# Kernel optimization log

Measured on AMD Instinct MI355X. Metric: run time of the kernel, lower is better.

The kernel has to match this reference:

```python
import jax, jax.numpy as jnp
import numpy as np

DEGREE = 8
HIDDEN = 256
IN_DIM = 3
N_LAYERS = 8  # num_hidden_layers=8 -> 1 input + 6 middle + 1 output ChebyKAN layers


def cheby_layer(x, coeff):
    """x: [P, in], coeff: [in, out, degree+1] -> [P, out].
    Computes tanh(x), Chebyshev recurrence T_0..T_d, and contracts
    sum_d T_d(x)_i * coeff[i, o, d] without materializing the full basis.
    """
    x = jnp.tanh(x)
    t_prev = jnp.ones_like(x)          # T_0
    t_cur = x                          # T_1
    out = jnp.einsum('pi,io->po', t_prev, coeff[:, :, 0])
    out = out + jnp.einsum('pi,io->po', t_cur, coeff[:, :, 1])
    for d in range(2, coeff.shape[-1]):
        t_prev, t_cur = t_cur, 2.0 * x * t_cur - t_prev
        out = out + jnp.einsum('pi,io->po', t_cur, coeff[:, :, d])
    return out


def decode(pts, ws):
    h = pts
    for w in ws:
        h = cheby_layer(h, w)
    return h


def setup_inputs() -> dict:
    key = jax.random.key(0)
    k_nm, k_m, *k_ws = jax.random.split(key, 2 + N_LAYERS)
    B, N = 4, 16384
    inp = {
        'non_mnfld_pnts': jax.random.normal(k_nm, (B, N, IN_DIM), dtype=jnp.float32),
        'mnfld_pnts': jax.random.normal(k_m, (B, N, IN_DIM), dtype=jnp.float32),
    }
    dims = [IN_DIM] + [HIDDEN] * (N_LAYERS - 1) + [1]
    for i in range(N_LAYERS):
        fan_in, fan_out = dims[i], dims[i + 1]
        std = 1.0 / (fan_in * (DEGREE + 1))
        inp[f'w{i}'] = jax.random.normal(k_ws[i], (fan_in, fan_out, DEGREE + 1), dtype=jnp.float32) * std
    return inp


def reference(non_mnfld_pnts, mnfld_pnts, w0, w1, w2, w3, w4, w5, w6, w7):
    ws = [w0, w1, w2, w3, w4, w5, w6, w7]
    B = non_mnfld_pnts.shape[0]
    mnfld_pred = decode(mnfld_pnts.reshape(-1, IN_DIM), ws).reshape(B, -1)
    nonmnfld_pred = decode(non_mnfld_pnts.reshape(-1, IN_DIM), ws).reshape(B, -1)
    return (mnfld_pred, nonmnfld_pred)
```

## Files before the change

kernel.cpp:

```cpp
#include <hip/hip_runtime.h>

typedef _Float16 f16;
typedef __attribute__((ext_vector_type(4)))  _Float16 f16x4;
typedef __attribute__((ext_vector_type(8)))  _Float16 f16x8;
typedef __attribute__((ext_vector_type(16))) float    f32x16;

#define WT_L (8*256*256)

__device__ __forceinline__ float fexp2(float x) {
#if __has_builtin(__builtin_amdgcn_exp2f)
    return __builtin_amdgcn_exp2f(x);
#else
    return exp2f(x);
#endif
}

__device__ __forceinline__ float fast_tanh(float v) {
    float a = __builtin_fabsf(v);
    float e = fexp2(a * -2.8853900817779268f);
    float r = (1.0f - e) * __builtin_amdgcn_rcpf(1.0f + e);
    return __builtin_copysignf(r, v);
}

__global__ void prep_all(const float* __restrict__ w0, const float* __restrict__ w1,
                         const float* __restrict__ w2, const float* __restrict__ w3,
                         const float* __restrict__ w4, const float* __restrict__ w5,
                         const float* __restrict__ w6, const float* __restrict__ w7,
                         f16* __restrict__ wt, float* __restrict__ biasp,
                         float* __restrict__ w0t, float* __restrict__ w7p)
{
    __shared__ float red[256];
    const int bi = blockIdx.x, t = threadIdx.x;
    if (bi < 1536) {
        const int L = bi >> 8, o = bi & 255, i = t;
        const float* w;
        switch (L) { case 0: w = w1; break; case 1: w = w2; break; case 2: w = w3; break;
                     case 3: w = w4; break; case 4: w = w5; break; default: w = w6; }
        float v[9];
#pragma unroll
        for (int d = 0; d < 9; d++) v[d] = w[(i*256 + o)*9 + d];
        const int ck = i >> 4, k = i & 15;
        const int wv4 = o >> 6, nt = (o >> 5) & 1, l31 = o & 31;
        const int lane = (k >> 3)*32 + l31, e = k & 7;
        const int base = ck*4096 + wv4*1024 + nt*512 + lane*8 + e;
#pragma unroll
        for (int d = 1; d < 9; d++)
            wt[L*WT_L + (d-1)*16*4096 + base] = (f16)v[d];
        red[i] = v[0];
        __syncthreads();
#pragma unroll
        for (int s = 128; s > 0; s >>= 1) {
            if (i < s) red[i] += red[i + s];
            __syncthreads();
        }
        if (i == 0) biasp[L*256 + o] = red[0];
    } else if (bi < 1563) {
        int id = (bi - 1536)*256 + t;
        int i = id / 2304, rem = id % 2304;
        int o = rem / 9, d = rem % 9;
        w0t[(i*9 + d)*256 + o] = w0[id];
    } else {
        int id = (bi - 1563)*256 + t;
        int ch = id / 9, d = id % 9;
        w7p[ch*12 + d] = w7[id];
    }
}

__global__ void k0(const float* __restrict__ nonm, const float* __restrict__ mnf,
                   const float* __restrict__ w0t, f16* __restrict__ xg) {
    const int t = threadIdx.x, b = blockIdx.x;
    const int pt = t & 63;
    const int oh = (t >> 6) * 64;
    const int pid = b*64 + pt;
    const float* src = (pid < 65536) ? mnf : nonm;
    const int sp = (pid < 65536) ? pid : pid - 65536;
    float c0 = src[sp*3 + 0];
    float c1 = src[sp*3 + 1];
    float c2 = src[sp*3 + 2];
    float xx[3] = {fast_tanh(c0), fast_tanh(c1), fast_tanh(c2)};
    float bas[27];
#pragma unroll
    for (int i = 0; i < 3; i++) {
        float t0 = 1.0f, t1 = xx[i];
        bas[i*9+0] = t0; bas[i*9+1] = t1;
        float x2 = xx[i] + xx[i];
#pragma unroll
        for (int d = 2; d < 9; d++) {
            float t2 = x2*t1 - t0;
            bas[i*9+d] = t2; t0 = t1; t1 = t2;
        }
    }
#pragma unroll 1
    for (int q = 0; q < 16; q++) {
        int o = oh + q*4;
        float4 a = {0.f, 0.f, 0.f, 0.f};
#pragma unroll
        for (int k = 0; k < 27; k++) {
            float4 wv = *(const float4*)(w0t + k*256 + o);
            a.x = fmaf(bas[k], wv.x, a.x);
            a.y = fmaf(bas[k], wv.y, a.y);
            a.z = fmaf(bas[k], wv.z, a.z);
            a.w = fmaf(bas[k], wv.w, a.w);
        }
        f16x4 hv = {(f16)fast_tanh(a.x), (f16)fast_tanh(a.y),
                    (f16)fast_tanh(a.z), (f16)fast_tanh(a.w)};
        *(f16x4*)(xg + (size_t)pid*256 + o) = hv;
    }
}

__global__ __launch_bounds__(256, 2)
void k_mid(const f16* __restrict__ wl, const float* __restrict__ biasL,
           f16* __restrict__ xg)
{
    __shared__ __align__(16) f16 xs[128*256];

    const int t    = threadIdx.x;
    const int b    = blockIdx.x;
    const int lane = t & 63;
    const int w    = t >> 6;
    const int l31  = lane & 31;
    const int half = lane >> 5;
    const int nb   = w * 64;
    const size_t tile_off = (size_t)b * 128 * 256;

#pragma unroll
    for (int i = 0; i < 16; i++) {
        int idx = i*256 + t;
        int pt = idx >> 5, cu = idx & 31;
        f16x8 v = *(const f16x8*)(xg + tile_off + (size_t)idx*8);
        *(f16x8*)(xs + pt*256 + ((cu ^ (pt & 7))*8)) = v;
    }
    __syncthreads();

    f32x16 acc[4][2];
    const f16x8 ones = {(f16)1.f,(f16)1.f,(f16)1.f,(f16)1.f,(f16)1.f,(f16)1.f,(f16)1.f,(f16)1.f};

    const f16* wbase = wl + w*1024 + lane*8;
    float b0 = biasL[nb + l31];
    float b1 = biasL[nb + 32 + l31];
#pragma unroll
    for (int mt = 0; mt < 4; mt++)
#pragma unroll
        for (int r = 0; r < 16; r++) { acc[mt][0][r] = b0; acc[mt][1][r] = b1; }

    f16x8 xv[4], Bb[4][2];
#pragma unroll
    for (int mt = 0; mt < 4; mt++) {
        int m = mt*32 + l31;
        int unit = half ^ (m & 7);
        xv[mt] = *(const f16x8*)(xs + m*256 + unit*8);
    }
#pragma unroll
    for (int j = 0; j < 4; j++) {
        Bb[j][0] = *(const f16x8*)(wbase + j*16*4096);
        Bb[j][1] = *(const f16x8*)(wbase + j*16*4096 + 512);
    }

    f16x8 x2[4], t1[4], t0[4];
#pragma unroll 1
    for (int ck = 0; ck < 16; ck++) {
        const int ckn = (ck < 15) ? ck + 1 : 15;
#pragma unroll
        for (int mt = 0; mt < 4; mt++) {
            t1[mt] = xv[mt];
            x2[mt] = xv[mt] + xv[mt];
            t0[mt] = ones;
        }
#pragma unroll
        for (int mt = 0; mt < 4; mt++) {
            int m = mt*32 + l31;
            int unit = (ckn*2 + half) ^ (m & 7);
            xv[mt] = *(const f16x8*)(xs + m*256 + unit*8);
        }
#pragma unroll
        for (int j = 0; j < 8; j++) {
            const int ck2 = (j < 4) ? ck : ckn;
            const int j2  = (j < 4) ? (j + 4) : (j - 4);
            const int off = (j2*16 + ck2)*4096;
            f16x8 pb0 = *(const f16x8*)(wbase + off);
            f16x8 pb1 = *(const f16x8*)(wbase + off + 512);
#pragma unroll
            for (int mt = 0; mt < 4; mt++) {
                acc[mt][0] = __builtin_amdgcn_mfma_f32_32x32x16_f16(t1[mt], Bb[j&3][0], acc[mt][0], 0, 0, 0);
                acc[mt][1] = __builtin_amdgcn_mfma_f32_32x32x16_f16(t1[mt], Bb[j&3][1], acc[mt][1], 0, 0, 0);
            }
            if (j < 7) {
#pragma unroll
                for (int mt = 0; mt < 4; mt++) {
                    f16x8 tn = x2[mt]*t1[mt] - t0[mt];
                    t0[mt] = t1[mt];
                    t1[mt] = tn;
                }
            }
            Bb[j&3][0] = pb0;
            Bb[j&3][1] = pb1;
        }
    }
    __syncthreads();

#pragma unroll
    for (int mt = 0; mt < 4; mt++) {
#pragma unroll
        for (int nt = 0; nt < 2; nt++) {
            int ch = nb + nt*32 + l31;
            int cu = ch >> 3, ce = ch & 7;
#pragma unroll
            for (int r = 0; r < 16; r++) {
                int p = mt*32 + (r & 3) + 8*(r >> 2) + 4*half;
                int unit = cu ^ (p & 7);
                xs[p*256 + unit*8 + ce] = (f16)fast_tanh(acc[mt][nt][r]);
            }
        }
    }
    __syncthreads();

#pragma unroll
    for (int i = 0; i < 16; i++) {
        int idx = i*256 + t;
        int pt = idx >> 5, cu = idx & 31;
        f16x8 v = *(const f16x8*)(xs + pt*256 + ((cu ^ (pt & 7))*8));
        *(f16x8*)(xg + tile_off + (size_t)idx*8) = v;
    }
}

__global__ void k7(const f16* __restrict__ xg, const float* __restrict__ w7p,
                   float* __restrict__ out) {
    __shared__ float w7s[256*12];
    const int t = threadIdx.x, b = blockIdx.x;
#pragma unroll
    for (int i = 0; i < 12; i++) w7s[i*256 + t] = w7p[i*256 + t];
    __syncthreads();
    const int pid = b*256 + t;
    const f16* row = xg + (size_t)pid*256;
    float s = 0.0f;
#pragma unroll 1
    for (int cu = 0; cu < 32; cu++) {
        f16x8 xv = *(const f16x8*)(row + cu*8);
#pragma unroll
        for (int e = 0; e < 8; e++) {
            int ch = cu*8 + e;
            const float* wr = w7s + ch*12;
            float x = (float)xv[e];
            float x2 = x + x;
            float t0 = 1.0f, t1v = x;
            s = fmaf(wr[0], t0, s);
            s = fmaf(wr[1], t1v, s);
            float t2 = x2*t1v - t0;  s = fmaf(wr[2], t2, s);
            float t3 = x2*t2 - t1v;  s = fmaf(wr[3], t3, s);
            float t4 = x2*t3 - t2;   s = fmaf(wr[4], t4, s);
            float t5 = x2*t4 - t3;   s = fmaf(wr[5], t5, s);
            float t6 = x2*t5 - t4;   s = fmaf(wr[6], t6, s);
            float t7 = x2*t6 - t5;   s = fmaf(wr[7], t7, s);
            float t8 = x2*t7 - t6;   s = fmaf(wr[8], t8, s);
        }
    }
    out[pid] = s;
}

extern "C" void kernel_launch(void* const* d_in, const int* in_sizes, int n_in,
                              void* d_out, int out_size, void* d_ws, size_t ws_size,
                              hipStream_t stream) {
    const float* nonm = (const float*)d_in[0];
    const float* mnf  = (const float*)d_in[1];

    char* ws = (char*)d_ws;
    f16*   wtp   = (f16*)ws;
    float* biasp = (float*)(ws + 6*WT_L*2);
    float* w0tp  = (float*)(ws + 6*WT_L*2 + 6144);
    float* w7pp  = (float*)(ws + 6*WT_L*2 + 6144 + 27648);
    f16*   xg    = (f16*)(ws + 6*WT_L*2 + 6144 + 27648 + 12288);

    prep_all<<<1572, 256, 0, stream>>>((const float*)d_in[2], (const float*)d_in[3],
                                       (const float*)d_in[4], (const float*)d_in[5],
                                       (const float*)d_in[6], (const float*)d_in[7],
                                       (const float*)d_in[8], (const float*)d_in[9],
                                       wtp, biasp, w0tp, w7pp);

    k0<<<2048, 256, 0, stream>>>(nonm, mnf, w0tp, xg);
    for (int L = 0; L < 6; L++)
        k_mid<<<1024, 256, 0, stream>>>(wtp + L*WT_L, biasp + L*256, xg);
    k7<<<512, 256, 0, stream>>>(xg, w7pp, (float*)d_out);
}
```

Before: 1.003 ms.

## Stream mid-layer weights through LDS with async global_load_lds and coalesce k0 stores

New measurement: 1.114 ms. 11.0% more time.

```diff
diff --git a/kernel.cpp b/kernel.cpp
--- a/kernel.cpp
+++ b/kernel.cpp
@@ -6,6 +6,15 @@
 typedef __attribute__((ext_vector_type(16))) float    f32x16;
 
 #define WT_L (8*256*256)
+
+#define WAIT_VM2   0x0F72
+#define WAIT_VM0   0x0F70
+#define WAIT_LGKM0 0xC07F
+
+__device__ __forceinline__ void async_b16(const f16* g, f16* l) {
+    __builtin_amdgcn_global_load_lds((const __attribute__((address_space(1))) void*)g,
+                                     (__attribute__((address_space(3))) void*)l, 16, 0, 0);
+}
 
 __device__ __forceinline__ float fexp2(float x) {
 #if __has_builtin(__builtin_amdgcn_exp2f)
@@ -68,6 +77,7 @@
 
 __global__ void k0(const float* __restrict__ nonm, const float* __restrict__ mnf,
                    const float* __restrict__ w0t, f16* __restrict__ xg) {
+    __shared__ __align__(16) f16 sh[64*256];
     const int t = threadIdx.x, b = blockIdx.x;
     const int pt = t & 63;
     const int oh = (t >> 6) * 64;
@@ -104,8 +114,21 @@
         }
         f16x4 hv = {(f16)fast_tanh(a.x), (f16)fast_tanh(a.y),
                     (f16)fast_tanh(a.z), (f16)fast_tanh(a.w)};
-        *(f16x4*)(xg + (size_t)pid*256 + o) = hv;
-    }
+        int unit = (o >> 3) ^ (pt & 7);
+        *(f16x4*)(sh + pt*256 + unit*8 + (o & 7)) = hv;
+    }
+    __syncthreads();
+#pragma unroll
+    for (int i = 0; i < 8; i++) {
+        int idx = i*256 + t;
+        int p2 = idx >> 5, cu = idx & 31;
+        f16x8 v = *(const f16x8*)(sh + p2*256 + ((cu ^ (p2 & 7))*8));
+        *(f16x8*)(xg + (size_t)b*16384 + (size_t)idx*8) = v;
+    }
+}
+
+__device__ __forceinline__ int goff(int s) {
+    return ((s & 7)*16 + (s >> 3)) * 4096;
 }
 
 __global__ __launch_bounds__(256, 2)
@@ -113,6 +136,7 @@
            f16* __restrict__ xg)
 {
     __shared__ __align__(16) f16 xs[128*256];
+    __shared__ __align__(16) f16 bring[2*4*1024];
 
     const int t    = threadIdx.x;
     const int b    = blockIdx.x;
@@ -121,7 +145,7 @@
     const int l31  = lane & 31;
     const int half = lane >> 5;
     const int nb   = w * 64;
-    const size_t tile_off = (size_t)b * 128 * 256;
+    const size_t tile_off = (size_t)b * 32768;
 
 #pragma unroll
     for (int i = 0; i < 16; i++) {
@@ -135,7 +159,10 @@
     f32x16 acc[4][2];
     const f16x8 ones = {(f16)1.f,(f16)1.f,(f16)1.f,(f16)1.f,(f16)1.f,(f16)1.f,(f16)1.f,(f16)1.f};
 
-    const f16* wbase = wl + w*1024 + lane*8;
+    const f16* wgl = wl + w*1024 + lane*8;
+    f16* lws = bring + w*1024;
+    const f16* lrd = bring + w*1024 + lane*8;
+
     float b0 = biasL[nb + l31];
     float b1 = biasL[nb + 32 + l31];
 #pragma unroll
@@ -143,28 +170,43 @@
 #pragma unroll
         for (int r = 0; r < 16; r++) { acc[mt][0][r] = b0; acc[mt][1][r] = b1; }
 
-    f16x8 xv[4], Bb[4][2];
+    f16x8 Bf[4][2];
+    async_b16(wgl + goff(0),       lws);
+    async_b16(wgl + goff(0) + 512, lws + 512);
+    async_b16(wgl + goff(1),       lws + 4096);
+    async_b16(wgl + goff(1) + 512, lws + 4096 + 512);
+    __builtin_amdgcn_s_waitcnt(WAIT_VM2);
+    __builtin_amdgcn_sched_barrier(0);
+    Bf[0][0] = *(const f16x8*)(lrd);
+    Bf[0][1] = *(const f16x8*)(lrd + 512);
+    __builtin_amdgcn_s_waitcnt(WAIT_VM0);
+    __builtin_amdgcn_sched_barrier(0);
+    Bf[1][0] = *(const f16x8*)(lrd + 4096);
+    Bf[1][1] = *(const f16x8*)(lrd + 4096 + 512);
+    __builtin_amdgcn_s_waitcnt(WAIT_LGKM0);
+    __builtin_amdgcn_sched_barrier(0);
+    async_b16(wgl + goff(2),       lws);
+    async_b16(wgl + goff(2) + 512, lws + 512);
+    async_b16(wgl + goff(3),       lws + 4096);
+    async_b16(wgl + goff(3) + 512, lws + 4096 + 512);
+
+    f16x8 xv[4];
 #pragma unroll
     for (int mt = 0; mt < 4; mt++) {
         int m = mt*32 + l31;
         int unit = half ^ (m & 7);
         xv[mt] = *(const f16x8*)(xs + m*256 + unit*8);
     }
-#pragma unroll
-    for (int j = 0; j < 4; j++) {
-        Bb[j][0] = *(const f16x8*)(wbase + j*16*4096);
-        Bb[j][1] = *(const f16x8*)(wbase + j*16*4096 + 512);
-    }
-
-    f16x8 x2[4], t1[4], t0[4];
+
+    f16x8 x2[4], t1[4], t0v[4];
 #pragma unroll 1
     for (int ck = 0; ck < 16; ck++) {
         const int ckn = (ck < 15) ? ck + 1 : 15;
 #pragma unroll
         for (int mt = 0; mt < 4; mt++) {
-            t1[mt] = xv[mt];
-            x2[mt] = xv[mt] + xv[mt];
-            t0[mt] = ones;
+            t1[mt]  = xv[mt];
+            x2[mt]  = xv[mt] + xv[mt];
+            t0v[mt] = ones;
         }
 #pragma unroll
         for (int mt = 0; mt < 4; mt++) {
@@ -173,27 +215,37 @@
             xv[mt] = *(const f16x8*)(xs + m*256 + unit*8);
         }
 #pragma unroll
-        for (int j = 0; j < 8; j++) {
-            const int ck2 = (j < 4) ? ck : ckn;
-            const int j2  = (j < 4) ? (j + 4) : (j - 4);
-            const int off = (j2*16 + ck2)*4096;
-            f16x8 pb0 = *(const f16x8*)(wbase + off);
-            f16x8 pb1 = *(const f16x8*)(wbase + off + 512);
+        for (int dm = 0; dm < 8; dm++) {
+            const int s = ck*8 + dm;
+            if (s + 2 < 128) {
+                __builtin_amdgcn_s_waitcnt(WAIT_VM2);
+                __builtin_amdgcn_sched_barrier(0);
+                const f16* rs = lrd + (dm & 1)*4096;
+                Bf[(dm+2)&3][0] = *(const f16x8*)(rs);
+                Bf[(dm+2)&3][1] = *(const f16x8*)(rs + 512);
+            }
 #pragma unroll
             for (int mt = 0; mt < 4; mt++) {
-                acc[mt][0] = __builtin_amdgcn_mfma_f32_32x32x16_f16(t1[mt], Bb[j&3][0], acc[mt][0], 0, 0, 0);
-                acc[mt][1] = __builtin_amdgcn_mfma_f32_32x32x16_f16(t1[mt], Bb[j&3][1], acc[mt][1], 0, 0, 0);
-            }
-            if (j < 7) {
+                acc[mt][0] = __builtin_amdgcn_mfma_f32_32x32x16_f16(t1[mt], Bf[dm&3][0], acc[mt][0], 0, 0, 0);
+                acc[mt][1] = __builtin_amdgcn_mfma_f32_32x32x16_f16(t1[mt], Bf[dm&3][1], acc[mt][1], 0, 0, 0);
+            }
+            if (dm < 7) {
 #pragma unroll
                 for (int mt = 0; mt < 4; mt++) {
-                    f16x8 tn = x2[mt]*t1[mt] - t0[mt];
-                    t0[mt] = t1[mt];
-                    t1[mt] = tn;
+                    f16x8 tn = x2[mt]*t1[mt] - t0v[mt];
+                    t0v[mt] = t1[mt];
+                    t1[mt]  = tn;
                 }
             }
-            Bb[j&3][0] = pb0;
-            Bb[j&3][1] = pb1;
+            if (s + 4 < 128) {
+                __builtin_amdgcn_s_waitcnt(WAIT_LGKM0);
+                __builtin_amdgcn_sched_barrier(0);
+                const int u = s + 4;
+                f16* ld = lws + (dm & 1)*4096;
+                const f16* g = wgl + goff(u);
+                async_b16(g,       ld);
+                async_b16(g + 512, ld + 512);
+            }
         }
     }
     __syncthreads();
```

## Stage k0 and k7 activations through swizzled LDS for coalesced access

Applied to the files above, without the earlier changes.

Measured after the change: 1.071 ms. +6.8%, slower.

```diff
diff --git a/kernel.cpp b/kernel.cpp
--- a/kernel.cpp
+++ b/kernel.cpp
@@ -68,6 +68,7 @@
 
 __global__ void k0(const float* __restrict__ nonm, const float* __restrict__ mnf,
                    const float* __restrict__ w0t, f16* __restrict__ xg) {
+    __shared__ __align__(16) f16 sh[64*256];
     const int t = threadIdx.x, b = blockIdx.x;
     const int pt = t & 63;
     const int oh = (t >> 6) * 64;
@@ -104,7 +105,16 @@
         }
         f16x4 hv = {(f16)fast_tanh(a.x), (f16)fast_tanh(a.y),
                     (f16)fast_tanh(a.z), (f16)fast_tanh(a.w)};
-        *(f16x4*)(xg + (size_t)pid*256 + o) = hv;
+        int unit = (o >> 3) ^ (pt & 7);
+        *(f16x4*)(sh + pt*256 + unit*8 + (o & 7)) = hv;
+    }
+    __syncthreads();
+#pragma unroll
+    for (int i = 0; i < 8; i++) {
+        int idx = i*256 + t;
+        int p2 = idx >> 5, cu = idx & 31;
+        f16x8 v = *(const f16x8*)(sh + p2*256 + ((cu ^ (p2 & 7))*8));
+        *(f16x8*)(xg + (size_t)b*16384 + (size_t)idx*8) = v;
     }
 }
 
@@ -121,7 +131,7 @@
     const int l31  = lane & 31;
     const int half = lane >> 5;
     const int nb   = w * 64;
-    const size_t tile_off = (size_t)b * 128 * 256;
+    const size_t tile_off = (size_t)b * 32768;
 
 #pragma unroll
     for (int i = 0; i < 16; i++) {
@@ -156,21 +166,14 @@
         Bb[j][1] = *(const f16x8*)(wbase + j*16*4096 + 512);
     }
 
-    f16x8 x2[4], t1[4], t0[4];
+    f16x8 t1[4], t0v[4];
 #pragma unroll 1
     for (int ck = 0; ck < 16; ck++) {
         const int ckn = (ck < 15) ? ck + 1 : 15;
 #pragma unroll
         for (int mt = 0; mt < 4; mt++) {
-            t1[mt] = xv[mt];
-            x2[mt] = xv[mt] + xv[mt];
-            t0[mt] = ones;
-        }
-#pragma unroll
-        for (int mt = 0; mt < 4; mt++) {
-            int m = mt*32 + l31;
-            int unit = (ckn*2 + half) ^ (m & 7);
-            xv[mt] = *(const f16x8*)(xs + m*256 + unit*8);
+            t1[mt]  = xv[mt];
+            t0v[mt] = ones;
         }
 #pragma unroll
         for (int j = 0; j < 8; j++) {
@@ -187,9 +190,17 @@
             if (j < 7) {
 #pragma unroll
                 for (int mt = 0; mt < 4; mt++) {
-                    f16x8 tn = x2[mt]*t1[mt] - t0[mt];
-                    t0[mt] = t1[mt];
-                    t1[mt] = tn;
+                    f16x8 tn = xv[mt]*(t1[mt] + t1[mt]) - t0v[mt];
+                    t0v[mt] = t1[mt];
+                    t1[mt]  = tn;
+                }
+            }
+            if (j == 6) {
+#pragma unroll
+                for (int mt = 0; mt < 4; mt++) {
+                    int m = mt*32 + l31;
+                    int unit = (ckn*2 + half) ^ (m & 7);
+                    xv[mt] = *(const f16x8*)(xs + m*256 + unit*8);
                 }
             }
             Bb[j&3][0] = pb0;
@@ -225,36 +236,52 @@
 
 __global__ void k7(const f16* __restrict__ xg, const float* __restrict__ w7p,
                    float* __restrict__ out) {
-    __shared__ float w7s[256*12];
+    __shared__ __align__(16) f16 sh[128*256];
     const int t = threadIdx.x, b = blockIdx.x;
-#pragma unroll
-    for (int i = 0; i < 12; i++) w7s[i*256 + t] = w7p[i*256 + t];
-    __syncthreads();
-    const int pid = b*256 + t;
-    const f16* row = xg + (size_t)pid*256;
+    const size_t tile_off = (size_t)b * 32768;
+#pragma unroll
+    for (int i = 0; i < 16; i++) {
+        int idx = i*256 + t;
+        int pt = idx >> 5, cu = idx & 31;
+        f16x8 v = *(const f16x8*)(xg + tile_off + (size_t)idx*8);
+        *(f16x8*)(sh + pt*256 + ((cu ^ (pt & 7))*8)) = v;
+    }
+    __syncthreads();
+
+    const int pt = t & 127;
+    const int seg = t >> 7;
     float s = 0.0f;
 #pragma unroll 1
-    for (int cu = 0; cu < 32; cu++) {
-        f16x8 xv = *(const f16x8*)(row + cu*8);
+    for (int q = 0; q < 16; q++) {
+        int u = seg*16 + q;
+        int unit = u ^ (pt & 7);
+        f16x8 xv = *(const f16x8*)(sh + pt*256 + unit*8);
 #pragma unroll
         for (int e = 0; e < 8; e++) {
-            int ch = cu*8 + e;
-            const float* wr = w7s + ch*12;
+            int ch = u*8 + e;
+            const float* wr = w7p + ch*12;
             float x = (float)xv[e];
+            float4 wa = *(const float4*)(wr);
+            float4 wb = *(const float4*)(wr + 4);
+            float wc = wr[8];
             float x2 = x + x;
             float t0 = 1.0f, t1v = x;
-            s = fmaf(wr[0], t0, s);
-            s = fmaf(wr[1], t1v, s);
-            float t2 = x2*t1v - t0;  s = fmaf(wr[2], t2, s);
-            float t3 = x2*t2 - t1v;  s = fmaf(wr[3], t3, s);
-            float t4 = x2*t3 - t2;   s = fmaf(wr[4], t4, s);
-            float t5 = x2*t4 - t3;   s = fmaf(wr[5], t5, s);
-            float t6 = x2*t5 - t4;   s = fmaf(wr[6], t6, s);
-            float t7 = x2*t6 - t5;   s = fmaf(wr[7], t7, s);
-            float t8 = x2*t7 - t6;   s = fmaf(wr[8], t8, s);
-        }
-    }
-    out[pid] = s;
+            s = fmaf(wa.x, t0, s);
+            s = fmaf(wa.y, t1v, s);
+            float t2 = x2*t1v - t0;  s = fmaf(wa.z, t2, s);
+            float t3 = x2*t2 - t1v;  s = fmaf(wa.w, t3, s);
+            float t4 = x2*t3 - t2;   s = fmaf(wb.x, t4, s);
+            float t5 = x2*t4 - t3;   s = fmaf(wb.y, t5, s);
+            float t6 = x2*t5 - t4;   s = fmaf(wb.z, t6, s);
+            float t7 = x2*t6 - t5;   s = fmaf(wb.w, t7, s);
+            float t8 = x2*t7 - t6;   s = fmaf(wc,  t8, s);
+        }
+    }
+    __syncthreads();
+    float* red = (float*)sh;
+    red[seg*128 + pt] = s;
+    __syncthreads();
+    if (t < 128) out[b*128 + t] = red[t] + red[128 + t];
 }
 
 extern "C" void kernel_launch(void* const* d_in, const int* in_sizes, int n_in,
@@ -279,5 +306,5 @@
     k0<<<2048, 256, 0, stream>>>(nonm, mnf, w0tp, xg);
     for (int L = 0; L < 6; L++)
         k_mid<<<1024, 256, 0, stream>>>(wtp + L*WT_L, biasp + L*256, xg);
-    k7<<<512, 256, 0, stream>>>(xg, w7pp, (float*)d_out);
-}
+    k7<<<1024, 256, 0, stream>>>(xg, w7pp, (float*)d_out);
+}
```
